# Optimization experiments

Measured on AMD Instinct MI355X. Metric: run time of the kernel, lower is better.

Reference implementation:

```python
import jax, jax.numpy as jnp
import numpy as np

S, D, H, G, DH = 2048, 4096, 32, 8, 128  # seq, d_in, heads, kv_groups, head_dim
GROUP = H // G


def rotate_half(x):
    x1, x2 = jnp.split(x, 2, axis=-1)
    return jnp.concatenate([-x2, x1], axis=-1)


def setup_inputs() -> dict:
    key = jax.random.key(0)
    ks = jax.random.split(key, 8)
    x = jax.random.normal(ks[0], (1, S, D), dtype=jnp.float32)
    # causal mask: True above the diagonal (positions to mask out)
    mask = jnp.triu(jnp.ones((S, S), dtype=bool), k=1)
    # standard RoPE tables
    inv_freq = 1.0 / (10000.0 ** (np.arange(0, DH, 2, dtype=np.float32) / DH))
    t = np.arange(S, dtype=np.float32)
    freqs = np.outer(t, inv_freq)                      # [S, DH/2]
    emb = np.concatenate([freqs, freqs], axis=-1)      # [S, DH]
    cos = jnp.asarray(np.cos(emb), dtype=jnp.float32)
    sin = jnp.asarray(np.sin(emb), dtype=jnp.float32)
    sc = 0.02
    Wq = jax.random.normal(ks[1], (D, H * DH), dtype=jnp.float32) * sc
    Wk = jax.random.normal(ks[2], (D, G * DH), dtype=jnp.float32) * sc
    Wv = jax.random.normal(ks[3], (D, G * DH), dtype=jnp.float32) * sc
    Wo = jax.random.normal(ks[4], (H * DH, D), dtype=jnp.float32) * sc
    return {"x": x, "mask": mask, "cos": cos, "sin": sin,
            "Wq": Wq, "Wk": Wk, "Wv": Wv, "Wo": Wo}


def reference(x, mask, cos, sin, Wq, Wk, Wv, Wo):
    xs = x[0]                                          # [S, D] (batch must be 1)
    q = (xs @ Wq).reshape(S, H, DH).transpose(1, 0, 2)   # [H, S, DH]
    k = (xs @ Wk).reshape(S, G, DH).transpose(1, 0, 2)   # [G, S, DH]
    v = (xs @ Wv).reshape(S, G, DH).transpose(1, 0, 2)   # [G, S, DH]
    # RoPE
    q = q * cos[None] + rotate_half(q) * sin[None]
    k = k * cos[None] + rotate_half(k) * sin[None]
    # GQA: repeat KV groups to match query heads
    k = jnp.repeat(k, GROUP, axis=0)                   # [H, S, DH]
    v = jnp.repeat(v, GROUP, axis=0)                   # [H, S, DH]
    scores = jnp.einsum('hsd,htd->hst', q, k)          # [H, S, S]
    scores = jnp.where(mask[None], -jnp.inf, scores)
    scores = scores / jnp.sqrt(jnp.float32(DH))
    w = jax.nn.softmax(scores, axis=-1)
    ctx = jnp.einsum('hst,htd->hsd', w, v)             # [H, S, DH]
    ctx = ctx.transpose(1, 0, 2).reshape(S, H * DH)
    out = ctx @ Wo                                     # [S, D]
    return out[None]                                   # [1, S, D]
```

## Files before the change

kernel.cpp:

```cpp
#include <hip/hip_runtime.h>
#include <hip/hip_bf16.h>
#include <cstdint>
#include <cstddef>

#define S 2048
#define D 4096
#define H 32
#define G 8
#define DH 128
#define HD (H*DH)
#define GD (G*DH)

typedef __bf16 bf16;
typedef __bf16 bf16x4 __attribute__((ext_vector_type(4)));
typedef __bf16 bf16x8 __attribute__((ext_vector_type(8)));
typedef float f32x4 __attribute__((ext_vector_type(4)));

__device__ __forceinline__ void gload16(const void* g, void* l) {
    __builtin_amdgcn_global_load_lds(
        (const __attribute__((address_space(1))) void*)g,
        (__attribute__((address_space(3))) void*)l, 16, 0, 0);
}

#define FENCE() asm volatile("" ::: "memory")
#define BARRIER() do { FENCE(); __builtin_amdgcn_s_barrier(); FENCE(); } while (0)
#define VMCNT(n)  asm volatile("s_waitcnt vmcnt(" #n ")" ::: "memory")
#define LGKM0()   do { asm volatile("s_waitcnt lgkmcnt(0)" ::: "memory"); \
                       __builtin_amdgcn_sched_barrier(0); } while (0)

__global__ __launch_bounds__(256) void prep_fused(
    const float* __restrict__ x, bf16* __restrict__ xb,
    const float* __restrict__ Wq, const float* __restrict__ Wk,
    const float* __restrict__ Wv, const float* __restrict__ Wo,
    bf16* __restrict__ Wqkvt, bf16* __restrict__ Wot)
{
    const int b = blockIdx.x, tid = threadIdx.x;
    if (b < 512) {
        int i = b * 4096 + tid;
        #pragma unroll
        for (int it = 0; it < 16; ++it, i += 256) {
            float4 v = reinterpret_cast<const float4*>(x)[i];
            bf16x4 o = { (bf16)v.x, (bf16)v.y, (bf16)v.z, (bf16)v.w };
            reinterpret_cast<bf16x4*>(xb)[i] = o;
        }
        return;
    }
    const float* in; bf16* out; int Cc, bx, by;
    if (b < 1536)      { int tb = b - 512;  in = Wq; out = Wqkvt;                       Cc = HD; bx = tb & 15; by = tb >> 4; }
    else if (b < 1792) { int tb = b - 1536; in = Wk; out = Wqkvt + (size_t)HD * D;      Cc = GD; bx = tb & 3;  by = tb >> 2; }
    else if (b < 2048) { int tb = b - 1792; in = Wv; out = Wqkvt + (size_t)(HD+GD) * D; Cc = GD; bx = tb & 3;  by = tb >> 2; }
    else               { int tb = b - 2048; in = Wo; out = Wot;                         Cc = D;  bx = tb & 15; by = tb >> 4; }
    const int r0 = by * 64 + (tid & 7) * 8;
    const int c0 = bx * 256 + (tid >> 3) * 8;
    bf16 m[8][8];
    #pragma unroll
    for (int j = 0; j < 8; ++j) {
        const float* p = in + (size_t)(r0 + j) * Cc + c0;
        float4 a = *reinterpret_cast<const float4*>(p);
        float4 bq = *reinterpret_cast<const float4*>(p + 4);
        m[j][0] = (bf16)a.x;  m[j][1] = (bf16)a.y;  m[j][2] = (bf16)a.z;  m[j][3] = (bf16)a.w;
        m[j][4] = (bf16)bq.x; m[j][5] = (bf16)bq.y; m[j][6] = (bf16)bq.z; m[j][7] = (bf16)bq.w;
    }
    #pragma unroll
    for (int i = 0; i < 8; ++i) {
        bf16x8 ov;
        #pragma unroll
        for (int j = 0; j < 8; ++j) ov[j] = m[j][i];
        *reinterpret_cast<bf16x8*>(out + (size_t)(c0 + i) * D + r0) = ov;
    }
}

__global__ __launch_bounds__(256) void rope_vt_fused(
    bf16* __restrict__ Qb, bf16* __restrict__ Kb,
    const bf16* __restrict__ Vb, bf16* __restrict__ VtG,
    const float* __restrict__ cosT, const float* __restrict__ sinT, float qs)
{
    const int b = blockIdx.x, tid = threadIdx.x;
    if (b < 20480) {
        bf16* Y; int ncols, idx; float scale;
        if (b < 16384) { Y = Qb; ncols = HD; idx = b * 256 + tid;           scale = qs; }
        else           { Y = Kb; ncols = GD; idx = (b - 16384) * 256 + tid; scale = 1.0f; }
        int pairs = ncols >> 1;
        int s = idx / pairs;
        int p = idx - s * pairs;
        int head = p >> 6;
        int d = p & 63;
        size_t base = (size_t)s * ncols + head * DH;
        float c  = cosT[s * DH + d];
        float sn = sinT[s * DH + d];
        float a = (float)Y[base + d];
        float bb = (float)Y[base + d + 64];
        Y[base + d]      = (bf16)((a * c - bb * sn) * scale);
        Y[base + d + 64] = (bf16)((bb * c + a * sn) * scale);
        return;
    }
    const int tb = b - 20480;
    const int r0 = (tb >> 2) * 64 + (tid & 7) * 8;
    const int c0 = (tb & 3) * 256 + (tid >> 3) * 8;
    bf16 m[8][8];
    #pragma unroll
    for (int j = 0; j < 8; ++j) {
        bf16x8 v = *reinterpret_cast<const bf16x8*>(Vb + (size_t)(r0 + j) * GD + c0);
        #pragma unroll
        for (int i = 0; i < 8; ++i) m[j][i] = v[i];
    }
    #pragma unroll
    for (int i = 0; i < 8; ++i) {
        bf16x8 ov;
        #pragma unroll
        for (int j = 0; j < 8; ++j) ov[j] = m[j][i];
        *reinterpret_cast<bf16x8*>(VtG + (size_t)(c0 + i) * S + r0) = ov;
    }
}

__global__ __launch_bounds__(256) void cast_f32_bf16(const float* __restrict__ in,
                                                     bf16* __restrict__ out, int n4)
{
    int i = blockIdx.x * 256 + threadIdx.x;
    if (i < n4) {
        float4 v = reinterpret_cast<const float4*>(in)[i];
        bf16x4 o = { (bf16)v.x, (bf16)v.y, (bf16)v.z, (bf16)v.w };
        reinterpret_cast<bf16x4*>(out)[i] = o;
    }
}

template<bool IN_F32>
__global__ __launch_bounds__(256) void transpose_to_bf16(
    const void* __restrict__ in, bf16* __restrict__ out, int R, int C)
{
    const int r0 = blockIdx.y * 64 + (threadIdx.x & 7) * 8;
    const int c0 = blockIdx.x * 256 + (threadIdx.x >> 3) * 8;
    bf16 m[8][8];
    #pragma unroll
    for (int j = 0; j < 8; ++j) {
        if constexpr (IN_F32) {
            const float* p = (const float*)in + (size_t)(r0 + j) * C + c0;
            float4 a = *reinterpret_cast<const float4*>(p);
            float4 b = *reinterpret_cast<const float4*>(p + 4);
            m[j][0] = (bf16)a.x; m[j][1] = (bf16)a.y; m[j][2] = (bf16)a.z; m[j][3] = (bf16)a.w;
            m[j][4] = (bf16)b.x; m[j][5] = (bf16)b.y; m[j][6] = (bf16)b.z; m[j][7] = (bf16)b.w;
        } else {
            const bf16* p = (const bf16*)in + (size_t)(r0 + j) * C + c0;
            bf16x8 v = *reinterpret_cast<const bf16x8*>(p);
            #pragma unroll
            for (int i = 0; i < 8; ++i) m[j][i] = v[i];
        }
    }
    #pragma unroll
    for (int i = 0; i < 8; ++i) {
        bf16x8 ov;
        #pragma unroll
        for (int j = 0; j < 8; ++j) ov[j] = m[j][i];
        *reinterpret_cast<bf16x8*>(out + (size_t)(c0 + i) * R + r0) = ov;
    }
}

__global__ __launch_bounds__(256) void rope_inplace(bf16* __restrict__ Y,
                                                    const float* __restrict__ cosT,
                                                    const float* __restrict__ sinT,
                                                    int ncols, int total, float scale)
{
    int idx = blockIdx.x * 256 + threadIdx.x;
    if (idx >= total) return;
    int pairs = ncols >> 1;
    int s = idx / pairs;
    int p = idx - s * pairs;
    int head = p >> 6;
    int d = p & 63;
    size_t base = (size_t)s * ncols + head * DH;
    float c  = cosT[s * DH + d];
    float sn = sinT[s * DH + d];
    float a = (float)Y[base + d];
    float b = (float)Y[base + d + 64];
    Y[base + d]      = (bf16)((a * c - b * sn) * scale);
    Y[base + d + 64] = (bf16)((b * c + a * sn) * scale);
}

__global__ __launch_bounds__(512) void gemm192q(
    const bf16* __restrict__ A, const bf16* __restrict__ Bt,
    bf16* __restrict__ Qout, bf16* __restrict__ Kout, bf16* __restrict__ Vout, int K)
{
    extern __shared__ char smem[];
    const int tid = threadIdx.x, lane = tid & 63, wave = tid >> 6;
    const int wr = wave >> 2, wc = wave & 3;
    const int l15 = lane & 15, lhi = lane >> 4;
    const int r8 = lane >> 3, c8 = lane & 7;
    const int csw = ((c8 ^ r8) << 3);

    const int x = blockIdx.x & 7, bi = blockIdx.x >> 3;
    const int brow = (x >> 2) * 4 + (bi & 3);
    const int bcol = (x & 3) * 8 + (bi >> 2);
    const int bm = brow * 256, bn = bcol * 192;
    const int NT = K >> 6;

    auto stA = [&](int buf, int h, int L, int t) {
        int row0 = L * 128 + h * 64 + wave * 8;
        gload16(A + (size_t)(bm + row0 + r8) * K + (t << 6) + csw,
                smem + buf * 57344 + row0 * 128);
    };
    auto stB = [&](int buf, int u, int t) {
        int row0 = u * 64 + wave * 8;
        gload16(Bt + (size_t)(bn + row0 + r8) * K + (t << 6) + csw,
                smem + buf * 57344 + 32768 + row0 * 128);
    };
    auto rdA = [&](const char* Cb, int mh, int ks, bf16x8* af) {
        #pragma unroll
        for (int m = 0; m < 4; ++m) {
            int row = wr * 128 + mh * 64 + m * 16 + l15;
            int ch = (ks * 4 + lhi) ^ (l15 & 7);
            af[m] = *reinterpret_cast<const bf16x8*>(Cb + row * 128 + ch * 16);
        }
    };
    auto rdB = [&](const char* Cb, int ks, bf16x8* bfv) {
        #pragma unroll
        for (int n = 0; n < 3; ++n) {
            int row = wc * 48 + n * 16 + l15;
            int ch = (ks * 4 + lhi) ^ (l15 & 7);
            bfv[n] = *reinterpret_cast<const bf16x8*>(Cb + 32768 + row * 128 + ch * 16);
        }
    };

    f32x4 acc[8][3] = {};
    auto mm = [&](int mh, const bf16x8* af, const bf16x8* bfv) {
        LGKM0();
        __builtin_amdgcn_s_setprio(1);
        #pragma unroll
        for (int m = 0; m < 4; ++m)
            #pragma unroll
            for (int n = 0; n < 3; ++n)
                acc[mh * 4 + m][n] = __builtin_amdgcn_mfma_f32_16x16x32_bf16(
                    af[m], bfv[n], acc[mh * 4 + m][n], 0, 0, 0);
        __builtin_amdgcn_s_setprio(0);
    };

    stB(0, 0, 0); stB(0, 1, 0); stB(0, 2, 0);
    stA(0, 0, 0, 0); stA(0, 0, 1, 0);
    stA(0, 1, 0, 0); stA(0, 1, 1, 0);
    VMCNT(2);
    BARRIER();

    for (int t = 0; t < NT; ++t) {
        const char* cur = smem + (t & 1) * 57344;
        const int nb = (t + 1) & 1;
        const int tn = (t + 1 < NT) ? t + 1 : t;
        bf16x8 af[4], bk0[3], bk1[3];

        rdA(cur, 0, 0, af); rdB(cur, 0, bk0);
        stB(nb, 0, tn); stB(nb, 1, tn);
        mm(0, af, bk0);
        BARRIER();

        rdA(cur, 0, 1, af); rdB(cur, 1, bk1);
        stB(nb, 2, tn); stA(nb, 0, 0, tn);
        mm(0, af, bk1);
        VMCNT(4);
        BARRIER();

        rdA(cur, 1, 0, af);
        stA(nb, 0, 1, tn); stA(nb, 1, 0, tn);
        mm(1, af, bk0);
        BARRIER();

        rdA(cur, 1, 1, af);
        stA(nb, 1, 1, tn);
        mm(1, af, bk1);
        VMCNT(2);
        BARRIER();
    }

    #pragma unroll
    for (int mm_i = 0; mm_i < 8; ++mm_i) {
        int r0 = bm + wr * 128 + (mm_i >> 2) * 64 + (mm_i & 3) * 16 + lhi * 4;
        #pragma unroll
        for (int n = 0; n < 3; ++n) {
            int c = bn + wc * 48 + n * 16 + l15;
            #pragma unroll
            for (int j = 0; j < 4; ++j) {
                bf16 v = (bf16)acc[mm_i][n][j];
                if (c < HD)            Qout[(size_t)(r0 + j) * HD + c] = v;
                else if (c < HD + GD)  Kout[(size_t)(r0 + j) * GD + (c - HD)] = v;
                else                   Vout[(size_t)(r0 + j) * GD + (c - HD - GD)] = v;
            }
        }
    }
}

__global__ __launch_bounds__(512, 2) void gemm3b(
    const bf16* __restrict__ A, const bf16* __restrict__ Bt,
    float* __restrict__ C, int N, int K)
{
    extern __shared__ char smem[];
    const int tid = threadIdx.x, lane = tid & 63, wave = tid >> 6;
    const int wr = wave >> 1, wc = wave & 1;
    const int l15 = lane & 15, lhi = lane >> 4;
    const int r8 = lane >> 3, c8 = lane & 7;
    const int csw = ((c8 ^ r8) << 3);

    const int x = blockIdx.x & 7, i = blockIdx.x >> 3;
    const int brow = (x >> 2) * 4 + (i & 3);
    const int bcol = (x & 3) * 8 + (i >> 2);
    const int bm = brow * 256, bn = bcol * 128;
    const int NT = K >> 6;

    auto stageA = [&](int buf, int L, int t) {
        int row0 = L * 64 + wave * 8;
        gload16(A + (size_t)(bm + row0 + r8) * K + (t << 6) + csw,
                smem + buf * 49152 + row0 * 128);
    };
    auto stageB = [&](int buf, int L, int t) {
        int row0 = L * 64 + wave * 8;
        gload16(Bt + (size_t)(bn + row0 + r8) * K + (t << 6) + csw,
                smem + buf * 49152 + 32768 + row0 * 128);
    };
    auto rdA = [&](const char* Ab, int ks, bf16x8* af) {
        #pragma unroll
        for (int m = 0; m < 4; ++m) {
            int row = wr * 64 + m * 16 + l15;
            int ch = (ks * 4 + lhi) ^ (l15 & 7);
            af[m] = *reinterpret_cast<const bf16x8*>(Ab + row * 128 + ch * 16);
        }
    };
    auto rdB = [&](const char* Bb, int ks, bf16x8* bfv) {
        #pragma unroll
        for (int n = 0; n < 4; ++n) {
            int row = wc * 64 + n * 16 + l15;
            int ch = (ks * 4 + lhi) ^ (l15 & 7);
            bfv[n] = *reinterpret_cast<const bf16x8*>(Bb + row * 128 + ch * 16);
        }
    };

    f32x4 acc[4][4] = {};

    #pragma unroll
    for (int L = 0; L < 4; ++L) stageA(0, L, 0);
    stageB(0, 0, 0); stageB(0, 1, 0);
    #pragma unroll
    for (int L = 0; L < 4; ++L) stageA(1, L, (1 < NT) ? 1 : 0);
    stageB(1, 0, (1 < NT) ? 1 : 0); stageB(1, 1, (1 < NT) ? 1 : 0);
    VMCNT(6);
    BARRIER();

    for (int t = 0; t < NT; ++t) {
        const char* Ab = smem + (t % 3) * 49152;
        const char* Bb = Ab + 32768;
        const int b2 = (t + 2) % 3;
        const int st = (t + 2 < NT) ? t + 2 : NT - 1;
        bf16x8 af[4], bk[4];

        rdB(Bb, 0, bk); rdA(Ab, 0, af);
        stageA(b2, 0, st); stageA(b2, 1, st);
        LGKM0();
        __builtin_amdgcn_s_setprio(1);
        #pragma unroll
        for (int m = 0; m < 4; ++m)
            #pragma unroll
            for (int n = 0; n < 4; ++n)
                acc[m][n] = __builtin_amdgcn_mfma_f32_16x16x32_bf16(af[m], bk[n], acc[m][n], 0, 0, 0);
        __builtin_amdgcn_s_setprio(0);

        rdB(Bb, 1, bk); rdA(Ab, 1, af);
        stageA(b2, 2, st); stageA(b2, 3, st);
        stageB(b2, 0, st); stageB(b2, 1, st);
        LGKM0();
        __builtin_amdgcn_s_setprio(1);
        #pragma unroll
        for (int m = 0; m < 4; ++m)
            #pragma unroll
            for (int n = 0; n < 4; ++n)
                acc[m][n] = __builtin_amdgcn_mfma_f32_16x16x32_bf16(af[m], bk[n], acc[m][n], 0, 0, 0);
        __builtin_amdgcn_s_setprio(0);

        VMCNT(6);
        BARRIER();
    }

    #pragma unroll
    for (int m = 0; m < 4; ++m) {
        int r0 = bm + wr * 64 + m * 16 + lhi * 4;
        #pragma unroll
        for (int n = 0; n < 4; ++n) {
            int c = bn + wc * 64 + n * 16 + l15;
            #pragma unroll
            for (int j = 0; j < 4; ++j)
                C[(size_t)(r0 + j) * N + c] = acc[m][n][j];
        }
    }
}

#define BM 128
#define BN 128
#define BK 32
#define LDSK 40

template<bool OUT_BF16>
__global__ __launch_bounds__(256) void gemm_aBf16(
    const bf16* __restrict__ A,
    const float* __restrict__ B0, const float* __restrict__ B1,
    void* __restrict__ C0, void* __restrict__ C1,
    int M, int N, int K)
{
    __shared__ alignas(16) bf16 Al[BM][LDSK];
    __shared__ alignas(16) bf16 Bt[BN][LDSK];

    const float* __restrict__ B = blockIdx.z ? B1 : B0;
    void* __restrict__ C = blockIdx.z ? C1 : C0;

    const int tid  = threadIdx.x;
    const int lane = tid & 63;
    const int wave = tid >> 6;
    const int wm = (wave >> 1) * 64;
    const int wn = (wave & 1) * 64;
    const int bm = blockIdx.y * BM;
    const int bn = blockIdx.x * BN;
    const int l15 = lane & 15;
    const int lhi = lane >> 4;

    f32x4 acc[4][4] = {};

    for (int k0 = 0; k0 < K; k0 += BK) {
        #pragma unroll
        for (int it = 0; it < 2; ++it) {
            int idx = it * 256 + tid;
            int row = idx >> 2;
            int ko  = idx & 3;
            bf16x8 v = *reinterpret_cast<const bf16x8*>(
                A + (size_t)(bm + row) * K + k0 + ko * 8);
            *reinterpret_cast<bf16x8*>(&Al[row][ko * 8]) = v;
        }
        {
            int n = tid & 127;
            int kbase = (tid >> 7) * 8;
            const float* bp = B + (size_t)k0 * N + bn + n;
            #pragma unroll
            for (int half = 0; half < 2; ++half) {
                bf16x8 v;
                #pragma unroll
                for (int j = 0; j < 8; ++j)
                    v[j] = (bf16)bp[(size_t)(half * 16 + kbase + j) * N];
                *reinterpret_cast<bf16x8*>(&Bt[n][half * 16 + kbase]) = v;
            }
        }
        __syncthreads();

        bf16x8 af[4], bfv[4];
        #pragma unroll
        for (int m = 0; m < 4; ++m)
            af[m] = *reinterpret_cast<const bf16x8*>(&Al[wm + m * 16 + l15][lhi * 8]);
        #pragma unroll
        for (int n = 0; n < 4; ++n)
            bfv[n] = *reinterpret_cast<const bf16x8*>(&Bt[wn + n * 16 + l15][lhi * 8]);
        #pragma unroll
        for (int m = 0; m < 4; ++m)
            #pragma unroll
            for (int n = 0; n < 4; ++n)
                acc[m][n] = __builtin_amdgcn_mfma_f32_16x16x32_bf16(
                    af[m], bfv[n], acc[m][n], 0, 0, 0);
        __syncthreads();
    }

    #pragma unroll
    for (int m = 0; m < 4; ++m) {
        int r0 = bm + wm + m * 16 + lhi * 4;
        #pragma unroll
        for (int n = 0; n < 4; ++n) {
            int c = bn + wn + n * 16 + l15;
            #pragma unroll
            for (int j = 0; j < 4; ++j) {
                if constexpr (OUT_BF16)
                    reinterpret_cast<bf16*>(C)[(size_t)(r0 + j) * N + c] = (bf16)acc[m][n][j];
                else
                    reinterpret_cast<float*>(C)[(size_t)(r0 + j) * N + c] = acc[m][n][j];
            }
        }
    }
}

#define QBLK 128
#define KVBLK 64
#define NQT (S/QBLK)

template<bool MASK>
__device__ __forceinline__ void attn_tile(
    int t0, int q0w, int l15, int lhi,
    const bf16x8* qf, const char* Kl, const char* Vl, char* Plw,
    f32x4* o, float& m_i, float& l_i)
{
    f32x4 sc[4] = {};
    __builtin_amdgcn_s_setprio(1);
    #pragma unroll
    for (int n = 0; n < 4; ++n) {
        int row = n * 16 + l15;
        #pragma unroll
        for (int kk = 0; kk < 4; ++kk) {
            bf16x8 kf = *reinterpret_cast<const bf16x8*>(
                Kl + row * 256 + ((((kk * 4 + lhi)) ^ (l15 & 7)) << 4));
            sc[n] = __builtin_amdgcn_mfma_f32_16x16x32_bf16(kf, qf[kk], sc[n], 0, 0, 0);
        }
    }
    __builtin_amdgcn_s_setprio(0);

    const int qr = q0w + l15;
    float vals[16];
    #pragma unroll
    for (int n = 0; n < 4; ++n)
        #pragma unroll
        for (int j = 0; j < 4; ++j) {
            float v = sc[n][j];
            if constexpr (MASK) {
                int t = t0 + n * 16 + lhi * 4 + j;
                if (t > qr) v = -1e30f;
            }
            vals[n * 4 + j] = v;
        }

    float m8[8], m4[4];
    #pragma unroll
    for (int k = 0; k < 8; ++k) m8[k] = fmaxf(vals[k], vals[k + 8]);
    #pragma unroll
    for (int k = 0; k < 4; ++k) m4[k] = fmaxf(m8[k], m8[k + 4]);
    float mx = fmaxf(fmaxf(m4[0], m4[1]), fmaxf(m4[2], m4[3]));
    mx = fmaxf(mx, __shfl_xor(mx, 16));
    mx = fmaxf(mx, __shfl_xor(mx, 32));

    const float mnew = (mx <= m_i + 8.0f) ? m_i : mx;
    const float cr = exp2f(m_i - mnew);

    float p[16];
    #pragma unroll
    for (int k = 0; k < 16; ++k) p[k] = exp2f(vals[k] - mnew);
    float s8[8], s4[4];
    #pragma unroll
    for (int k = 0; k < 8; ++k) s8[k] = p[k] + p[k + 8];
    #pragma unroll
    for (int k = 0; k < 4; ++k) s4[k] = s8[k] + s8[k + 4];
    float rsum = (s4[0] + s4[1]) + (s4[2] + s4[3]);
    rsum += __shfl_xor(rsum, 16);
    rsum += __shfl_xor(rsum, 32);
    l_i = l_i * cr + rsum;
    m_i = mnew;

    #pragma unroll
    for (int n = 0; n < 4; ++n) {
        bf16x4 w = { (bf16)p[n*4+0], (bf16)p[n*4+1], (bf16)p[n*4+2], (bf16)p[n*4+3] };
        int off = (l15 << 7) + (((n << 5) + (lhi << 3)) ^ ((l15 & 7) << 4));
        *reinterpret_cast<bf16x4*>(Plw + off) = w;
    }

    float corr[4];
    #pragma unroll
    for (int j = 0; j < 4; ++j) corr[j] = __shfl(cr, lhi * 4 + j, 16);
    if ((corr[0] != 1.f) | (corr[1] != 1.f) | (corr[2] != 1.f) | (corr[3] != 1.f)) {
        #pragma unroll
        for (int n = 0; n < 8; ++n)
            #pragma unroll
            for (int j = 0; j < 4; ++j)
                o[n][j] *= corr[j];
    }

    __builtin_amdgcn_s_setprio(1);
    #pragma unroll
    for (int kk = 0; kk < 2; ++kk) {
        bf16x8 pf = *reinterpret_cast<const bf16x8*>(
            Plw + (l15 << 7) + ((((kk * 4 + lhi)) ^ (l15 & 7)) << 4));
        #pragma unroll
        for (int n = 0; n < 8; ++n) {
            int d = n * 16 + l15;
            bf16x8 vf = *reinterpret_cast<const bf16x8*>(
                Vl + (d << 7) + ((((kk * 4 + lhi)) ^ (d & 7)) << 4));
            o[n] = __builtin_amdgcn_mfma_f32_16x16x32_bf16(pf, vf, o[n], 0, 0, 0);
        }
    }
    __builtin_amdgcn_s_setprio(0);
}

__global__ __launch_bounds__(512) void flash_fwd6(
    const bf16* __restrict__ Q, const bf16* __restrict__ Kr,
    const bf16* __restrict__ VtG, bf16* __restrict__ ctx)
{
    extern __shared__ char fsm[];

    const int tid  = threadIdx.x;
    const int lane = tid & 63;
    const int wave = tid >> 6;
    const int l15 = lane & 15;
    const int lhi = lane >> 4;
    const int bid = blockIdx.x;
    const int qt = (NQT - 1) - (bid >> 5);
    const int h  = ((bid & 7) << 2) | ((bid >> 3) & 3);
    const int g  = h >> 2;
    const int q0 = qt * QBLK;
    const int q0w = q0 + wave * 16;
    char* Plw = fsm + 65536 + wave * 2048;

    bf16x8 qf[4];
    {
        const bf16* qp = Q + (size_t)(q0w + l15) * HD + h * DH + lhi * 8;
        #pragma unroll
        for (int kk = 0; kk < 4; ++kk)
            qf[kk] = *reinterpret_cast<const bf16x8*>(qp + kk * 32);
    }

    f32x4 o[8] = {};
    float m_i = -1e30f;
    float l_i = 0.f;

    auto stage = [&](int t0, int buf) {
        char* Kl = fsm + buf * 32768;
        char* Vl = Kl + 16384;
        #pragma unroll
        for (int t = 0; t < 2; ++t) {
            int ch = t * 512 + tid;
            {
                int row = ch >> 4, ci = ch & 15;
                gload16(Kr + (size_t)(t0 + row) * GD + g * DH + ((ci ^ (row & 7)) << 3),
                        Kl + ch * 16);
            }
            {
                int d = ch >> 3, ci = ch & 7;
                gload16(VtG + (size_t)(g * DH + d) * S + t0 + ((ci ^ (d & 7)) << 3),
                        Vl + ch * 16);
            }
        }
    };

    const int nt = 2 * qt + 2;
    stage(0, 0);
    VMCNT(0);
    BARRIER();

    for (int it = 0; it < nt; ++it) {
        if (it + 1 < nt) stage((it + 1) * KVBLK, (it + 1) & 1);
        const char* Kl = fsm + (it & 1) * 32768;
        const char* Vl = Kl + 16384;
        if (it >= nt - 2)
            attn_tile<true>(it * KVBLK, q0w, l15, lhi, qf, Kl, Vl, Plw, o, m_i, l_i);
        else
            attn_tile<false>(it * KVBLK, q0w, l15, lhi, qf, Kl, Vl, Plw, o, m_i, l_i);
        VMCNT(0);
        BARRIER();
    }

    float lf[4];
    #pragma unroll
    for (int j = 0; j < 4; ++j) lf[j] = __shfl(l_i, lhi * 4 + j, 16);

    #pragma unroll
    for (int n = 0; n < 8; ++n) {
        int c = h * DH + n * 16 + l15;
        #pragma unroll
        for (int j = 0; j < 4; ++j) {
            int r = q0w + lhi * 4 + j;
            ctx[(size_t)r * HD + c] = (bf16)(o[n][j] / lf[j]);
        }
    }
}

extern "C" void kernel_launch(void* const* d_in, const int* in_sizes, int n_in,
                              void* d_out, int out_size, void* d_ws, size_t ws_size,
                              hipStream_t stream)
{
    const float* x    = (const float*)d_in[0];
    const float* cosT = (const float*)d_in[2];
    const float* sinT = (const float*)d_in[3];
    const float* Wq   = (const float*)d_in[4];
    const float* Wk   = (const float*)d_in[5];
    const float* Wv   = (const float*)d_in[6];
    const float* Wo   = (const float*)d_in[7];
    float* out = (float*)d_out;

    const size_t MB = (size_t)1 << 20;
    char* ws = (char*)d_ws;
    bf16* xb  = (bf16*)ws;
    bf16* ctx = (bf16*)(ws + 16 * MB);
    bf16* Qb  = (bf16*)d_out;
    bf16* Kb  = Qb + (size_t)S * HD;
    bf16* Vb  = Kb + (size_t)S * GD;
    bf16* VtG = Vb + (size_t)S * GD;

    const bool fast = ws_size >= 112 * MB;
    const float qscale = 0.08838834764831845f * 1.4426950408889634f;

    hipFuncSetAttribute(reinterpret_cast<const void*>(&flash_fwd6),
                        hipFuncAttributeMaxDynamicSharedMemorySize, 81920);

    if (fast) {
        bf16* Wqkvt = (bf16*)(ws + 32 * MB);
        bf16* Wot   = (bf16*)(ws + 80 * MB);

        hipFuncSetAttribute(reinterpret_cast<const void*>(&gemm192q),
                            hipFuncAttributeMaxDynamicSharedMemorySize, 114688);
        hipFuncSetAttribute(reinterpret_cast<const void*>(&gemm3b),
                            hipFuncAttributeMaxDynamicSharedMemorySize, 147456);

        prep_fused<<<3072, 256, 0, stream>>>(x, xb, Wq, Wk, Wv, Wo, Wqkvt, Wot);

        gemm192q<<<256, 512, 114688, stream>>>(xb, Wqkvt, Qb, Kb, Vb, D);

        rope_vt_fused<<<20608, 256, 0, stream>>>(Qb, Kb, Vb, VtG, cosT, sinT, qscale);

        flash_fwd6<<<NQT * H, 512, 81920, stream>>>(Qb, Kb, VtG, ctx);

        gemm3b<<<256, 512, 147456, stream>>>(ctx, Wot, out, D, HD);
    } else {
        cast_f32_bf16<<<(S * D / 4 + 255) / 256, 256, 0, stream>>>(x, xb, S * D / 4);

        gemm_aBf16<true><<<dim3(HD / BN, S / BM, 1), 256, 0, stream>>>(
            xb, Wq, Wq, (void*)Qb, (void*)Qb, S, HD, D);
        gemm_aBf16<true><<<dim3(GD / BN, S / BM, 2), 256, 0, stream>>>(
            xb, Wk, Wv, (void*)Kb, (void*)Vb, S, GD, D);

        rope_inplace<<<(S * HD / 2 + 255) / 256, 256, 0, stream>>>(Qb, cosT, sinT, HD, S * HD / 2, qscale);
        rope_inplace<<<(S * GD / 2 + 255) / 256, 256, 0, stream>>>(Kb, cosT, sinT, GD, S * GD / 2, 1.0f);

        transpose_to_bf16<false><<<dim3(GD / 256, S / 64), 256, 0, stream>>>(Vb, VtG, S, GD);

        flash_fwd6<<<NQT * H, 512, 81920, stream>>>(Qb, Kb, VtG, ctx);

        gemm_aBf16<false><<<dim3(D / BN, S / BM, 1), 256, 0, stream>>>(
            ctx, Wo, Wo, (void*)out, (void*)out, S, D, HD);
    }

    (void)in_sizes; (void)n_in; (void)out_size; (void)ws_size;
}
```

Measured before the change: 320.3 us.

## Move Wo cast/transpose into extra flash-attention blocks to overlap with attention

The Wo fp32→bf16 transpose moves out of the prep kernel and into 64 extra blocks appended to the flash attention launch. The causal attention grid has a long tail, and these blocks are meant to fill idle CUs there, hiding the weight conversion behind attention and shortening the prep kernel. The extra blocks each loop over 8 passes. Because they carry flash's 80KB shared memory reservation, they may compete for occupancy with attention blocks.

```diff
diff --git a/kernel.cpp b/kernel.cpp
--- a/kernel.cpp
+++ b/kernel.cpp
@@ -31,8 +31,7 @@
 __global__ __launch_bounds__(256) void prep_fused(
     const float* __restrict__ x, bf16* __restrict__ xb,
     const float* __restrict__ Wq, const float* __restrict__ Wk,
-    const float* __restrict__ Wv, const float* __restrict__ Wo,
-    bf16* __restrict__ Wqkvt, bf16* __restrict__ Wot)
+    const float* __restrict__ Wv, bf16* __restrict__ Wqkvt)
 {
     const int b = blockIdx.x, tid = threadIdx.x;
     if (b < 512) {
@@ -48,8 +47,7 @@
     const float* in; bf16* out; int Cc, bx, by;
     if (b < 1536)      { int tb = b - 512;  in = Wq; out = Wqkvt;                       Cc = HD; bx = tb & 15; by = tb >> 4; }
     else if (b < 1792) { int tb = b - 1536; in = Wk; out = Wqkvt + (size_t)HD * D;      Cc = GD; bx = tb & 3;  by = tb >> 2; }
-    else if (b < 2048) { int tb = b - 1792; in = Wv; out = Wqkvt + (size_t)(HD+GD) * D; Cc = GD; bx = tb & 3;  by = tb >> 2; }
-    else               { int tb = b - 2048; in = Wo; out = Wot;                         Cc = D;  bx = tb & 15; by = tb >> 4; }
+    else               { int tb = b - 1792; in = Wv; out = Wqkvt + (size_t)(HD+GD) * D; Cc = GD; bx = tb & 3;  by = tb >> 2; }
     const int r0 = by * 64 + (tid & 7) * 8;
     const int c0 = bx * 256 + (tid >> 3) * 8;
     bf16 m[8][8];
@@ -478,6 +476,7 @@
 #define QBLK 128
 #define KVBLK 64
 #define NQT (S/QBLK)
+#define FLASH_BLOCKS (NQT*H)
 
 template<bool MASK>
 __device__ __forceinline__ void attn_tile(
@@ -575,16 +574,44 @@
 
 __global__ __launch_bounds__(512) void flash_fwd6(
     const bf16* __restrict__ Q, const bf16* __restrict__ Kr,
-    const bf16* __restrict__ VtG, bf16* __restrict__ ctx)
+    const bf16* __restrict__ VtG, bf16* __restrict__ ctx,
+    const float* __restrict__ WoIn, bf16* __restrict__ WotOut)
 {
     extern __shared__ char fsm[];
 
     const int tid  = threadIdx.x;
+    const int bid = blockIdx.x;
+
+    if (bid >= FLASH_BLOCKS) {
+        const int tb = bid - FLASH_BLOCKS;
+        const int r0 = tb * 64 + (tid & 7) * 8;
+        #pragma unroll 1
+        for (int pass = 0; pass < 8; ++pass) {
+            const int c0 = pass * 512 + (tid >> 3) * 8;
+            bf16 m[8][8];
+            #pragma unroll
+            for (int j = 0; j < 8; ++j) {
+                const float* p = WoIn + (size_t)(r0 + j) * D + c0;
+                float4 a = *reinterpret_cast<const float4*>(p);
+                float4 b = *reinterpret_cast<const float4*>(p + 4);
+                m[j][0] = (bf16)a.x; m[j][1] = (bf16)a.y; m[j][2] = (bf16)a.z; m[j][3] = (bf16)a.w;
+                m[j][4] = (bf16)b.x; m[j][5] = (bf16)b.y; m[j][6] = (bf16)b.z; m[j][7] = (bf16)b.w;
+            }
+            #pragma unroll
+            for (int i = 0; i < 8; ++i) {
+                bf16x8 ov;
+                #pragma unroll
+                for (int j = 0; j < 8; ++j) ov[j] = m[j][i];
+                *reinterpret_cast<bf16x8*>(WotOut + (size_t)(c0 + i) * HD + r0) = ov;
+            }
+        }
+        return;
+    }
+
     const int lane = tid & 63;
     const int wave = tid >> 6;
     const int l15 = lane & 15;
     const int lhi = lane >> 4;
-    const int bid = blockIdx.x;
     const int qt = (NQT - 1) - (bid >> 5);
     const int h  = ((bid & 7) << 2) | ((bid >> 3) & 3);
     const int g  = h >> 2;
@@ -692,13 +719,14 @@
         hipFuncSetAttribute(reinterpret_cast<const void*>(&gemm3b),
                             hipFuncAttributeMaxDynamicSharedMemorySize, 147456);
 
-        prep_fused<<<3072, 256, 0, stream>>>(x, xb, Wq, Wk, Wv, Wo, Wqkvt, Wot);
+        prep_fused<<<2048, 256, 0, stream>>>(x, xb, Wq, Wk, Wv, Wqkvt);
 
         gemm192q<<<256, 512, 114688, stream>>>(xb, Wqkvt, Qb, Kb, Vb, D);
 
         rope_vt_fused<<<20608, 256, 0, stream>>>(Qb, Kb, Vb, VtG, cosT, sinT, qscale);
 
-        flash_fwd6<<<NQT * H, 512, 81920, stream>>>(Qb, Kb, VtG, ctx);
+        flash_fwd6<<<FLASH_BLOCKS + 64, 512, 81920, stream>>>(
+            Qb, Kb, VtG, ctx, Wo, Wot);
 
         gemm3b<<<256, 512, 147456, stream>>>(ctx, Wot, out, D, HD);
     } else {
@@ -714,7 +742,10 @@
 
         transpose_to_bf16<false><<<dim3(GD / 256, S / 64), 256, 0, stream>>>(Vb, VtG, S, GD);
 
-        flash_fwd6<<<NQT * H, 512, 81920, stream>>>(Qb, Kb, VtG, ctx);
+        float* dummyWot = nullptr; (void)dummyWot;
+        bf16* WotF = (bf16*)(ws + 0);
+        (void)WotF;
+        flash_fwd6<<<FLASH_BLOCKS, 512, 81920, stream>>>(Qb, Kb, VtG, ctx, Wo, (bf16*)ws);
 
         gemm_aBf16<false><<<dim3(D / BN, S / BM, 1), 256, 0, stream>>>(
             ctx, Wo, Wo, (void*)out, (void*)out, S, D, HD);
```

New measurement: 338.0 us. +5.5%, slower.
